# Optimization experiments

Hardware: AMD Instinct MI355X
Metric: run time of the kernel (lower is better)

The kernel has to match this reference:

```python
import jax, jax.numpy as jnp
import numpy as np
from jax import lax

ROUTING_ITERS = 3
EPS = 1e-8


def _conv(x, w, b, stride=1):
    # x: [B,C,H,W], w: [O,C,kh,kw]  (VALID padding, NCHW/OIHW)
    y = lax.conv_general_dilated(x, w, (stride, stride), 'VALID',
                                 dimension_numbers=('NCHW', 'OIHW', 'NCHW'))
    return y + b[None, :, None, None]


def _maxpool2(x):
    return lax.reduce_window(x, -jnp.inf, lax.max, (1, 1, 2, 2), (1, 1, 2, 2), 'VALID')


def _squash(s, axis=-1):
    n2 = jnp.sum(s * s, axis=axis, keepdims=True)
    return s * (n2 / (1.0 + n2)) / jnp.sqrt(n2 + EPS)


def setup_inputs() -> dict:
    key = jax.random.key(0)
    ks = jax.random.split(key, 9)
    p = lambda k, shp: (jax.random.normal(k, shp, dtype=jnp.float32) * 0.05)
    return {
        'x':  jax.random.normal(ks[0], (64, 1, 92, 92), dtype=jnp.float32),
        'w1': p(ks[1], (128, 1, 9, 9)),   'b1': jnp.zeros((128,), jnp.float32),
        'w2': p(ks[2], (64, 128, 5, 5)),  'b2': jnp.zeros((64,), jnp.float32),
        'wc': p(ks[3], (128, 64, 8, 8)),  'bc': jnp.zeros((128,), jnp.float32),
        # routing transform: [num_primary=1024, num_sar=10, out_dim=16, in_dim=32]
        'Wr': p(ks[4], (1024, 10, 16, 32)),
    }


def reference(x, w1, b1, w2, b2, wc, bc, Wr):
    B = x.shape[0]
    # feature extractor (dropout is identity at inference)
    h = jax.nn.relu(_conv(x, w1, b1))          # [B,128,84,84]
    h = _maxpool2(h)                            # [B,128,42,42]
    h = _conv(h, w2, b2)                        # [B,64,38,38]
    # primary capsule conv
    h = _conv(h, wc, bc, stride=2)              # [B,128,16,16]
    # 128 channels = 4 capsule types * 32-dim capsules, 16x16 spatial -> 1024 caps
    u = h.reshape(B, 4, 32, 16, 16).transpose(0, 1, 3, 4, 2).reshape(B, 1024, 32)
    u = _squash(u)                              # [B,1024,32]
    # u_hat: predictions of each primary cap for each SAR cap
    u_hat = jnp.einsum('bpi,ptoi->bpto', u, Wr)  # [B,1024,10,16]
    # dynamic routing
    b_log = jnp.zeros((B, 1024, 10), dtype=x.dtype)
    for _ in range(ROUTING_ITERS):
        c = jax.nn.softmax(b_log, axis=2)               # [B,1024,10]
        s = jnp.einsum('bpt,bpto->bto', c, u_hat)       # [B,10,16]
        v = _squash(s)                                   # [B,10,16]
        b_log = b_log + jnp.einsum('bpto,bto->bpt', u_hat, v)
    likelihood = jnp.sqrt(jnp.sum(v * v, axis=-1) + EPS)  # [B,10]
    return likelihood
```

## Files before the change

### kernel.cpp

```cpp
#include <hip/hip_runtime.h>
#include <hip/hip_bf16.h>
#include <math.h>


#define EPSF 1e-8f

typedef __bf16 bf16x8 __attribute__((ext_vector_type(8)));
typedef __bf16 bf16x4 __attribute__((ext_vector_type(4)));
typedef float floatx4 __attribute__((ext_vector_type(4)));
typedef float floatx16 __attribute__((ext_vector_type(16)));

__global__ __launch_bounds__(256) void k_t_all(const float* __restrict__ Wr,
                                               const float* __restrict__ wc,
                                               const float* __restrict__ w2,
                                               const float* __restrict__ w1,
                                               __bf16* __restrict__ wrb,
                                               __bf16* __restrict__ wca,
                                               __bf16* __restrict__ w2a,
                                               __bf16* __restrict__ w1b) {
    int i = blockIdx.x * 256 + threadIdx.x;
    if (i < 5242880) {
        int e = i & 7, l = (i >> 3) & 63;
        int pt_ = i >> 9;
        int o = l & 15, k = (l >> 4) * 8 + e;
        wrb[i] = (__bf16)Wr[((size_t)pt_ * 16 + o) * 32 + k];
        return;
    }
    int i2 = i - 5242880;
    if (i2 < 524288) {
        int j = i2 & 7, lane = (i2 >> 3) & 63, f = i2 >> 9;
        int ct = f & 3, ks = (f >> 2) & 1, khw = (f >> 3) & 63, icc = f >> 9;
        int c32 = lane & 31, h = lane >> 5;
        int oc = ct * 32 + c32;
        int ic = icc * 32 + ks * 16 + h * 8 + j;
        wca[i2] = (__bf16)wc[(oc * 64 + ic) * 64 + khw];
        return;
    }
    int i3 = i2 - 524288;
    if (i3 < 204800) {
        int j = i3 & 7, lane = (i3 >> 3) & 63, f = i3 >> 9;
        int mt = f & 1, ks = (f >> 1) & 3, rem = f >> 3;
        int khw = rem % 25, icc = rem / 25;
        int c32 = lane & 31, h = lane >> 5;
        int oc = mt * 32 + c32;
        int ic = icc * 64 + ks * 16 + h * 8 + j;
        w2a[i3] = (__bf16)w2[(oc * 128 + ic) * 25 + khw];
        return;
    }
    int i4 = i3 - 204800;
    if (i4 < 12288) {
        int kt = i4 >> 10, oc = (i4 >> 3) & 127, j = i4 & 7;
        int k = kt * 8 + j;
        w1b[i4] = (__bf16)(k < 81 ? w1[oc * 81 + k] : 0.f);
    }
}

__global__ __launch_bounds__(256, 3) void k_conv1_mfma(const float* __restrict__ x,
                                                       const __bf16* __restrict__ w1b,
                                                       const float* __restrict__ b1,
                                                       __bf16* __restrict__ h1n) {
    __shared__ float xs[960];
    __shared__ __bf16 Bl[18432];
    int py = blockIdx.x, b = blockIdx.y;
    int t = threadIdx.x;
    int lane = t & 63, w = t >> 6;
    int cc = lane & 15, q = lane >> 4;

    const float* xb = x + (size_t)b * 8464 + 2 * py * 92;
    for (int j = t; j < 920; j += 256) xs[j] = xb[j];

    bf16x8 af2[2][3];
#pragma unroll
    for (int g2 = 0; g2 < 2; ++g2)
#pragma unroll
        for (int ks = 0; ks < 3; ++ks)
            af2[g2][ks] = *(const bf16x8*)(w1b + ((ks * 4 + q) * 128 + g2 * 64 + w * 16 + cc) * 8);

    __syncthreads();

    if (t < 192) {
        int row = t / 96, pos = t - (t / 96) * 96;
        int sbase = row * 92 + pos;
        bool pvalid = pos < 84;
#pragma unroll
        for (int kt = 0; kt < 12; ++kt) {
            bf16x8 pk;
#pragma unroll
            for (int j = 0; j < 8; ++j) {
                int k = kt * 8 + j;
                int kh = k / 9, kw = k - kh * 9;
                float v = (pvalid && k < 81) ? xs[sbase + kh * 92 + kw] : 0.f;
                pk[j] = (__bf16)v;
            }
            *(bf16x8*)(Bl + ((kt * 2 + row) * 96 + pos) * 8) = pk;
        }
    }
    __syncthreads();

    floatx4 acc[2][2][6];
#pragma unroll
    for (int g2 = 0; g2 < 2; ++g2)
#pragma unroll
        for (int rr = 0; rr < 2; ++rr)
#pragma unroll
            for (int n6 = 0; n6 < 6; ++n6)
                acc[g2][rr][n6] = (floatx4){0.f, 0.f, 0.f, 0.f};

    const char* Bb = (const char*)Bl + cc * 16 + q * 3072;
#pragma unroll
    for (int rr = 0; rr < 2; ++rr)
#pragma unroll
        for (int n6 = 0; n6 < 6; ++n6) {
#pragma unroll
            for (int ks = 0; ks < 3; ++ks) {
                bf16x8 bf = *(const bf16x8*)(Bb + ks * 12288 + rr * 1536 + n6 * 256);
                acc[0][rr][n6] = __builtin_amdgcn_mfma_f32_16x16x32_bf16(af2[0][ks], bf, acc[0][rr][n6], 0, 0, 0);
                acc[1][rr][n6] = __builtin_amdgcn_mfma_f32_16x16x32_bf16(af2[1][ks], bf, acc[1][rr][n6], 0, 0, 0);
            }
        }

#pragma unroll
    for (int g2 = 0; g2 < 2; ++g2) {
        int oc0 = g2 * 64 + w * 16 + q * 4;
        float4 bv = *(const float4*)(b1 + oc0);
        size_t obase = (((size_t)b * 42 + py) * 42) * 128 + oc0;
#pragma unroll
        for (int n6 = 0; n6 < 6; ++n6) {
            bf16x4 pk;
#pragma unroll
            for (int r = 0; r < 4; ++r) {
                float vert = fmaxf(acc[g2][0][n6][r], acc[g2][1][n6][r]);
                float hz = fmaxf(vert, __shfl_xor(vert, 1, 64));
                float pooled = fmaxf(hz + ((const float*)&bv)[r], 0.f);
                pk[r] = (__bf16)pooled;
            }
            if ((cc & 1) == 0) {
                int px = n6 * 8 + (cc >> 1);
                if (px < 42)
                    *(bf16x4*)(h1n + obase + (size_t)px * 128) = pk;
            }
        }
    }
}

__global__ __launch_bounds__(256) void k_conv2(const __bf16* __restrict__ h1n,
                                               const __bf16* __restrict__ w2a,
                                               float* __restrict__ p01) {
    __shared__ __bf16 ins[25704];
    int g = blockIdx.x, b = blockIdx.y, icc = blockIdx.z;
    int row0 = g * 5;
    int t = threadIdx.x;
    int lane = t & 63, w = t >> 6;
    int c32 = lane & 31, h = lane >> 5;
    int validp = (g < 7) ? 190 : 114;
    int ic0 = icc * 64;

    int baseN[2], posi[2];
#pragma unroll
    for (int nt = 0; nt < 2; ++nt) {
        int pi = (w * 2 + nt) * 32 + c32;
        int pc = pi < validp ? pi : validp - 1;
        int r = pc / 38, c = pc - r * 38;
        posi[nt] = pi;
        baseN[nt] = (r * 42 + c) * 136 + h * 16;
    }

#pragma unroll
    for (int half = 0; half < 2; ++half) {
        uint4 rb[6];
        int lo[6];
#pragma unroll
        for (int k = 0; k < 6; ++k) {
            int j = (half * 6 + k) * 256 + t;
            if (j > 3023) j -= 256;
            int lr = j / 336, rem = j - lr * 336;
            int ix = rem >> 3, sb = rem & 7;
            int rg = row0 + lr; if (rg > 41) rg = 41;
            rb[k] = *(const uint4*)(h1n + ((((size_t)b * 42 + rg) * 42 + ix) * 128 + ic0 + sb * 8));
            lo[k] = (lr * 42 + ix) * 136 + sb * 16;
        }
#pragma unroll
        for (int k = 0; k < 6; ++k)
            *(uint4*)((char*)ins + lo[k]) = rb[k];
    }

    floatx16 acc[2][2];
#pragma unroll
    for (int mt = 0; mt < 2; ++mt)
#pragma unroll
        for (int nt = 0; nt < 2; ++nt)
#pragma unroll
            for (int i = 0; i < 16; ++i) acc[mt][nt][i] = 0.f;

    const __bf16* wic = w2a + (size_t)icc * 25 * 4096 + (lane << 3);

    bf16x8 abuf[3][8];
#pragma unroll
    for (int ks = 0; ks < 4; ++ks) {
        abuf[0][ks * 2]     = *(const bf16x8*)(wic + 0 * 4096 + ks * 1024);
        abuf[0][ks * 2 + 1] = *(const bf16x8*)(wic + 0 * 4096 + ks * 1024 + 512);
        abuf[1][ks * 2]     = *(const bf16x8*)(wic + 1 * 4096 + ks * 1024);
        abuf[1][ks * 2 + 1] = *(const bf16x8*)(wic + 1 * 4096 + ks * 1024 + 512);
    }

    __syncthreads();
#pragma unroll
    for (int khw = 0; khw < 25; ++khw) {
        if (khw + 2 < 25) {
            const __bf16* wk2 = wic + (khw + 2) * 4096;
#pragma unroll
            for (int ks = 0; ks < 4; ++ks) {
                abuf[(khw + 2) % 3][ks * 2]     = *(const bf16x8*)(wk2 + ks * 1024);
                abuf[(khw + 2) % 3][ks * 2 + 1] = *(const bf16x8*)(wk2 + ks * 1024 + 512);
            }
        }
        int kh = khw / 5, kw = khw - kh * 5;
        int doff = (kh * 42 + kw) * 136;
#pragma unroll
        for (int ks = 0; ks < 4; ++ks) {
            bf16x8 a0 = abuf[khw % 3][ks * 2];
            bf16x8 a1 = abuf[khw % 3][ks * 2 + 1];
#pragma unroll
            for (int nt = 0; nt < 2; ++nt) {
                bf16x8 bfr = *(const bf16x8*)((char*)ins + baseN[nt] + doff + ks * 32);
                acc[0][nt] = __builtin_amdgcn_mfma_f32_32x32x16_bf16(a0, bfr, acc[0][nt], 0, 0, 0);
                acc[1][nt] = __builtin_amdgcn_mfma_f32_32x32x16_bf16(a1, bfr, acc[1][nt], 0, 0, 0);
            }
        }
    }
    float* pdst = p01 + (size_t)icc * 5914624;
#pragma unroll
    for (int nt = 0; nt < 2; ++nt) {
        int pi = posi[nt];
        if (pi < validp) {
            int r = pi / 38, c = pi - r * 38;
            int oh = row0 + r;
            size_t obase = (((size_t)b * 38 + oh) * 38 + c) * 64;
#pragma unroll
            for (int mt = 0; mt < 2; ++mt) {
#pragma unroll
                for (int g2 = 0; g2 < 4; ++g2) {
                    int oc0 = mt * 32 + g2 * 8 + h * 4;
                    floatx4 pv;
                    pv[0] = acc[mt][nt][g2 * 4 + 0];
                    pv[1] = acc[mt][nt][g2 * 4 + 1];
                    pv[2] = acc[mt][nt][g2 * 4 + 2];
                    pv[3] = acc[mt][nt][g2 * 4 + 3];
                    *(floatx4*)(pdst + obase + oc0) = pv;
                }
            }
        }
    }
}

__global__ __launch_bounds__(256) void k_reduce_h2(const float* __restrict__ p01,
                                                   const float* __restrict__ b2,
                                                   __bf16* __restrict__ h2n) {
    int i = blockIdx.x * 256 + threadIdx.x;
    if (i >= 1478656) return;
    size_t e = (size_t)i * 4;
    floatx4 a = *(const floatx4*)(p01 + e);
    floatx4 b = *(const floatx4*)(p01 + 5914624 + e);
    floatx4 bv = *(const floatx4*)(b2 + ((i * 4) & 63));
    bf16x4 pk;
    pk.x = (__bf16)(a[0] + b[0] + bv[0]);
    pk.y = (__bf16)(a[1] + b[1] + bv[1]);
    pk.z = (__bf16)(a[2] + b[2] + bv[2]);
    pk.w = (__bf16)(a[3] + b[3] + bv[3]);
    *(bf16x4*)(h2n + e) = pk;
}

__global__ __launch_bounds__(256, 4) void k_convcaps(const __bf16* __restrict__ h2n,
                                                     const __bf16* __restrict__ wca,
                                                     float* __restrict__ pc) {
    __shared__ __bf16 ins[13680];
    int g = blockIdx.x, b = blockIdx.y, icc = blockIdx.z;
    int t = threadIdx.x;
    int lane = t & 63, ct = t >> 6;
    int c32 = lane & 31, h = lane >> 5;
    int rloc = c32 >> 4, cx = c32 & 15;
    int ic0 = icc * 32;

    floatx16 acc;
#pragma unroll
    for (int i = 0; i < 16; ++i) acc[i] = 0.f;

    int Bbase = (76 * rloc + cx) * 72 + h * 16;
    {
        uint4 rb[6];
        int lo[6];
#pragma unroll
        for (int k = 0; k < 6; ++k) {
            int j = k * 256 + t;
            if (j > 1519) j -= 256;
            int r = j / 152, rem = j - r * 152;
            int c = rem >> 2, s = rem & 3;
            rb[k] = *(const uint4*)(h2n + ((((size_t)b * 38 + 4 * g + r) * 38 + c) * 64 + ic0 + s * 8));
            int X = (r * 2 + (c & 1)) * 19 + (c >> 1);
            lo[k] = X * 72 + s * 16;
        }
#pragma unroll
        for (int k = 0; k < 6; ++k)
            *(uint4*)((char*)ins + lo[k]) = rb[k];
    }
    __syncthreads();
    const __bf16* wic = wca + ((size_t)icc * 64 * 8 + ct) * 512 + (lane << 3);
#pragma unroll
    for (int khw = 0; khw < 64; ++khw) {
        int kh = khw >> 3, kw = khw & 7;
        int par = kw & 1, k2 = kw >> 1;
        int doff = ((kh * 2 + par) * 19 + k2) * 72;
        const __bf16* wk = wic + khw * 4096;
#pragma unroll
        for (int ks = 0; ks < 2; ++ks) {
            bf16x8 af = *(const bf16x8*)(wk + ks * 2048);
            bf16x8 bfr = *(const bf16x8*)((char*)ins + Bbase + doff + ks * 32);
            acc = __builtin_amdgcn_mfma_f32_32x32x16_bf16(af, bfr, acc, 0, 0, 0);
        }
    }
    int pos = (2 * g + rloc) * 16 + cx;
    float* dst = pc + (size_t)icc * 2097152 + (((size_t)b * 1024 + ct * 256 + pos) * 32);
#pragma unroll
    for (int g2 = 0; g2 < 4; ++g2) {
        floatx4 pv;
        pv[0] = acc[g2 * 4 + 0];
        pv[1] = acc[g2 * 4 + 1];
        pv[2] = acc[g2 * 4 + 2];
        pv[3] = acc[g2 * 4 + 3];
        *(floatx4*)(dst + g2 * 8 + h * 4) = pv;
    }
}

__global__ __launch_bounds__(256) void k_squash(const float* __restrict__ pc,
                                                const float* __restrict__ bc,
                                                __bf16* __restrict__ ub) {
    int i = blockIdx.x * 256 + threadIdx.x;
    if (i >= 65536) return;
    int ct = (i >> 8) & 3;
    const float* p0 = pc + (size_t)i * 32;
    const float* p1 = pc + 2097152 + (size_t)i * 32;
    const float* bv = bc + ct * 32;
    float vals[32];
    float n2 = 0.f;
#pragma unroll
    for (int k = 0; k < 8; ++k) {
        floatx4 a = *(const floatx4*)(p0 + k * 4);
        floatx4 b = *(const floatx4*)(p1 + k * 4);
        floatx4 bb = *(const floatx4*)(bv + k * 4);
#pragma unroll
        for (int e = 0; e < 4; ++e) {
            float v = a[e] + b[e] + bb[e];
            vals[k * 4 + e] = v;
            n2 = fmaf(v, v, n2);
        }
    }
    float scale = (n2 / (1.f + n2)) / sqrtf(n2 + EPSF);
    __bf16* dst = ub + (size_t)i * 32;
#pragma unroll
    for (int k = 0; k < 8; ++k) {
        bf16x4 pk;
        pk.x = (__bf16)(vals[k * 4 + 0] * scale);
        pk.y = (__bf16)(vals[k * 4 + 1] * scale);
        pk.z = (__bf16)(vals[k * 4 + 2] * scale);
        pk.w = (__bf16)(vals[k * 4 + 3] * scale);
        *(bf16x4*)(dst + k * 4) = pk;
    }
}

__global__ __launch_bounds__(256) void k_uhat(const __bf16* __restrict__ ub,
                                              const __bf16* __restrict__ wrf,
                                              __bf16* __restrict__ uhT) {
    int pg = blockIdx.x, ts = blockIdx.y;
    int t = threadIdx.x;
    int lane = t & 63, bt = t >> 6;
    int bcol = bt * 16 + (lane & 15);
    int ko = lane >> 4;
    const __bf16* ubase = ub + (size_t)bcol * 32768 + ko * 8;
    __bf16* obase = uhT + ((size_t)bcol * 10 + ts) * 16384 + ko * 4;
#pragma unroll 4
    for (int i = 0; i < 16; ++i) {
        int p = pg * 16 + i;
        bf16x8 a = *(const bf16x8*)(wrf + (((size_t)p * 10 + ts) * 64 + lane) * 8);
        bf16x8 bb = *(const bf16x8*)(ubase + (size_t)p * 32);
        floatx4 c = (floatx4){0.f, 0.f, 0.f, 0.f};
        c = __builtin_amdgcn_mfma_f32_16x16x32_bf16(a, bb, c, 0, 0, 0);
        bf16x4 pk;
        pk.x = (__bf16)c[0];
        pk.y = (__bf16)c[1];
        pk.z = (__bf16)c[2];
        pk.w = (__bf16)c[3];
        *(bf16x4*)(obase + (size_t)p * 16) = pk;
    }
}

#define UHS_ADDR(P, HF) ((((P) << 5) + ((HF) << 4)) ^ ((((P) >> 2) & 7) << 4))
__global__ __launch_bounds__(256) void k_route(const __bf16* __restrict__ uhT,
                                               const float* __restrict__ blR,
                                               float* __restrict__ blW,
                                               float* __restrict__ out,
                                               int first, int dob, int last) {
    __shared__ __bf16 uh_s[16384];
    __shared__ float sred[4][16];
    __shared__ float vs[16];
    int b = blockIdx.x, tt = blockIdx.y;
    int t = threadIdx.x;
    const __bf16* uhb = uhT + ((size_t)b * 10 + tt) * 16384;
#pragma unroll
    for (int k = 0; k < 8; ++k) {
        int j = k * 256 + t;
        *(uint4*)((char*)uh_s + UHS_ADDR(j >> 1, j & 1)) =
            *(const uint4*)((const char*)uhb + j * 16);
    }
    __syncthreads();

    float acc[16];
#pragma unroll
    for (int o = 0; o < 16; ++o) acc[o] = 0.f;
    const float* blb = blR + b * 10240;
    for (int p = t; p < 1024; p += 256) {
        float c;
        if (first) {
            c = 0.1f;
        } else {
            float den = 0.f, et = 0.f;
#pragma unroll
            for (int tp = 0; tp < 10; ++tp) {
                float e = expf(blb[tp * 1024 + p]);
                den += e;
                if (tp == tt) et = e;
            }
            c = et / den;
        }
        bf16x8 u0 = *(const bf16x8*)((char*)uh_s + UHS_ADDR(p, 0));
        bf16x8 u1 = *(const bf16x8*)((char*)uh_s + UHS_ADDR(p, 1));
#pragma unroll
        for (int o = 0; o < 8; ++o) {
            acc[o]     = fmaf(c, (float)u0[o], acc[o]);
            acc[8 + o] = fmaf(c, (float)u1[o], acc[8 + o]);
        }
    }
    int lane = t & 63, wid = t >> 6;
#pragma unroll
    for (int o = 0; o < 16; ++o) {
        float v = acc[o];
#pragma unroll
        for (int off = 32; off >= 1; off >>= 1) v += __shfl_xor(v, off, 64);
        if (lane == 0) sred[wid][o] = v;
    }
    __syncthreads();
    if (t < 16) {
        float s = (sred[0][t] + sred[1][t]) + (sred[2][t] + sred[3][t]);
        float n2 = s * s;
#pragma unroll
        for (int off = 1; off < 16; off <<= 1) n2 += __shfl_xor(n2, off, 16);
        float scale = (n2 / (1.f + n2)) / sqrtf(n2 + EPSF);
        vs[t] = s * scale;
        if (last && t == 0) {
            float sv2 = n2 * scale * scale;
            out[b * 10 + tt] = sqrtf(sv2 + EPSF);
        }
    }
    __syncthreads();

    if (dob) {
        const float* blr = blR + (b * 10 + tt) * 1024;
        float* blw = blW + (b * 10 + tt) * 1024;
        for (int p = t; p < 1024; p += 256) {
            bf16x8 u0 = *(const bf16x8*)((char*)uh_s + UHS_ADDR(p, 0));
            bf16x8 u1 = *(const bf16x8*)((char*)uh_s + UHS_ADDR(p, 1));
            float d = 0.f;
#pragma unroll
            for (int o = 0; o < 8; ++o) {
                d = fmaf((float)u0[o], vs[o], d);
                d = fmaf((float)u1[o], vs[8 + o], d);
            }
            blw[p] = first ? d : (blr[p] + d);
        }
    }
}

extern "C" void kernel_launch(void* const* d_in, const int* in_sizes, int n_in,
                              void* d_out, int out_size, void* d_ws, size_t ws_size,
                              hipStream_t stream) {
    const float* x  = (const float*)d_in[0];
    const float* w1 = (const float*)d_in[1];
    const float* b1 = (const float*)d_in[2];
    const float* w2 = (const float*)d_in[3];
    const float* b2 = (const float*)d_in[4];
    const float* wc = (const float*)d_in[5];
    const float* bc = (const float*)d_in[6];
    const float* Wr = (const float*)d_in[7];
    float* out = (float*)d_out;
    float* ws  = (float*)d_ws;

    __bf16* w2a = (__bf16*)(ws);
    __bf16* wca = (__bf16*)(ws + 102400);
    __bf16* w1b = (__bf16*)(ws + 364544);
    __bf16* h1n = (__bf16*)(ws + 375040);
    __bf16* h2n = (__bf16*)(ws + 7600384);
    __bf16* ub  = (__bf16*)(ws + 12654848);
    float*  blA = ws + 14752000;
    __bf16* wrb = (__bf16*)(ws + 15417600);
    float*  p01 = ws + 18039040;
    float*  pc  = ws + 18039040;
    float*  blB = ws + 29868288;
    __bf16* uhT = (__bf16*)(ws + 375040);

    k_t_all<<<23376, 256, 0, stream>>>(Wr, wc, w2, w1, wrb, wca, w2a, w1b);
    k_conv1_mfma<<<dim3(42, 64), 256, 0, stream>>>(x, w1b, b1, h1n);
    k_conv2<<<dim3(8, 64, 2), 256, 0, stream>>>(h1n, w2a, p01);
    k_reduce_h2<<<5776, 256, 0, stream>>>(p01, b2, h2n);
    k_convcaps<<<dim3(8, 64, 2), 256, 0, stream>>>(h2n, wca, pc);
    k_squash<<<256, 256, 0, stream>>>(pc, bc, ub);
    k_uhat<<<dim3(64, 10), 256, 0, stream>>>(ub, wrb, uhT);
    k_route<<<dim3(64, 10), 256, 0, stream>>>(uhT, blA, blA, out, 1, 1, 0);
    k_route<<<dim3(64, 10), 256, 0, stream>>>(uhT, blA, blB, out, 0, 1, 0);
    k_route<<<dim3(64, 10), 256, 0, stream>>>(uhT, blB, blB, out, 0, 0, 1);
}
```

Baseline: 273.4 us.

## Fuse three routing iterations into one cooperative kernel with grid sync

Merges the three k_route launches into a single cooperative kernel that loads each block's u_hat slice into shared memory once and runs all three routing iterations, using a grid-wide sync between iterations to exchange the routing logits. This removes two kernel launches and two reloads of the 32KB u_hat tile per block. In exchange it requires all 640 blocks to be co-resident and adds grid barrier overhead. Correctness depends on the cooperative launch succeeding.

```diff
diff --git a/kernel.cpp b/kernel.cpp
--- a/kernel.cpp
+++ b/kernel.cpp
@@ -1,5 +1,6 @@
 #include <hip/hip_runtime.h>
 #include <hip/hip_bf16.h>
+#include <hip/hip_cooperative_groups.h>
 #include <math.h>
 
 
@@ -394,16 +395,17 @@
 }
 
 #define UHS_ADDR(P, HF) ((((P) << 5) + ((HF) << 4)) ^ ((((P) >> 2) & 7) << 4))
-__global__ __launch_bounds__(256) void k_route(const __bf16* __restrict__ uhT,
-                                               const float* __restrict__ blR,
-                                               float* __restrict__ blW,
-                                               float* __restrict__ out,
-                                               int first, int dob, int last) {
+__global__ __launch_bounds__(256) void k_route_all(const __bf16* __restrict__ uhT,
+                                                   float* __restrict__ blA,
+                                                   float* __restrict__ blB,
+                                                   float* __restrict__ out) {
+    cooperative_groups::grid_group gg = cooperative_groups::this_grid();
     __shared__ __bf16 uh_s[16384];
     __shared__ float sred[4][16];
     __shared__ float vs[16];
     int b = blockIdx.x, tt = blockIdx.y;
     int t = threadIdx.x;
+    int lane = t & 63, wid = t >> 6;
     const __bf16* uhb = uhT + ((size_t)b * 10 + tt) * 16384;
 #pragma unroll
     for (int k = 0; k < 8; ++k) {
@@ -413,68 +415,74 @@
     }
     __syncthreads();
 
-    float acc[16];
-#pragma unroll
-    for (int o = 0; o < 16; ++o) acc[o] = 0.f;
-    const float* blb = blR + b * 10240;
-    for (int p = t; p < 1024; p += 256) {
-        float c;
-        if (first) {
-            c = 0.1f;
-        } else {
-            float den = 0.f, et = 0.f;
-#pragma unroll
-            for (int tp = 0; tp < 10; ++tp) {
-                float e = expf(blb[tp * 1024 + p]);
-                den += e;
-                if (tp == tt) et = e;
-            }
-            c = et / den;
-        }
-        bf16x8 u0 = *(const bf16x8*)((char*)uh_s + UHS_ADDR(p, 0));
-        bf16x8 u1 = *(const bf16x8*)((char*)uh_s + UHS_ADDR(p, 1));
-#pragma unroll
-        for (int o = 0; o < 8; ++o) {
-            acc[o]     = fmaf(c, (float)u0[o], acc[o]);
-            acc[8 + o] = fmaf(c, (float)u1[o], acc[8 + o]);
-        }
-    }
-    int lane = t & 63, wid = t >> 6;
-#pragma unroll
-    for (int o = 0; o < 16; ++o) {
-        float v = acc[o];
-#pragma unroll
-        for (int off = 32; off >= 1; off >>= 1) v += __shfl_xor(v, off, 64);
-        if (lane == 0) sred[wid][o] = v;
-    }
-    __syncthreads();
-    if (t < 16) {
-        float s = (sred[0][t] + sred[1][t]) + (sred[2][t] + sred[3][t]);
-        float n2 = s * s;
-#pragma unroll
-        for (int off = 1; off < 16; off <<= 1) n2 += __shfl_xor(n2, off, 16);
-        float scale = (n2 / (1.f + n2)) / sqrtf(n2 + EPSF);
-        vs[t] = s * scale;
-        if (last && t == 0) {
-            float sv2 = n2 * scale * scale;
-            out[b * 10 + tt] = sqrtf(sv2 + EPSF);
-        }
-    }
-    __syncthreads();
-
-    if (dob) {
-        const float* blr = blR + (b * 10 + tt) * 1024;
-        float* blw = blW + (b * 10 + tt) * 1024;
+#pragma unroll 1
+    for (int it = 0; it < 3; ++it) {
+        const float* blR = (it == 1) ? blA : blB;
+        float acc[16];
+#pragma unroll
+        for (int o = 0; o < 16; ++o) acc[o] = 0.f;
+        const float* blb = blR + b * 10240;
         for (int p = t; p < 1024; p += 256) {
+            float c;
+            if (it == 0) {
+                c = 0.1f;
+            } else {
+                float den = 0.f, et = 0.f;
+#pragma unroll
+                for (int tp = 0; tp < 10; ++tp) {
+                    float e = expf(blb[tp * 1024 + p]);
+                    den += e;
+                    if (tp == tt) et = e;
+                }
+                c = et / den;
+            }
             bf16x8 u0 = *(const bf16x8*)((char*)uh_s + UHS_ADDR(p, 0));
             bf16x8 u1 = *(const bf16x8*)((char*)uh_s + UHS_ADDR(p, 1));
-            float d = 0.f;
 #pragma unroll
             for (int o = 0; o < 8; ++o) {
-                d = fmaf((float)u0[o], vs[o], d);
-                d = fmaf((float)u1[o], vs[8 + o], d);
-            }
-            blw[p] = first ? d : (blr[p] + d);
+                acc[o]     = fmaf(c, (float)u0[o], acc[o]);
+                acc[8 + o] = fmaf(c, (float)u1[o], acc[8 + o]);
+            }
+        }
+#pragma unroll
+        for (int o = 0; o < 16; ++o) {
+            float v = acc[o];
+#pragma unroll
+            for (int off = 32; off >= 1; off >>= 1) v += __shfl_xor(v, off, 64);
+            if (lane == 0) sred[wid][o] = v;
+        }
+        __syncthreads();
+        if (t < 16) {
+            float s = (sred[0][t] + sred[1][t]) + (sred[2][t] + sred[3][t]);
+            float n2 = s * s;
+#pragma unroll
+            for (int off = 1; off < 16; off <<= 1) n2 += __shfl_xor(n2, off, 16);
+            float scale = (n2 / (1.f + n2)) / sqrtf(n2 + EPSF);
+            vs[t] = s * scale;
+            if (it == 2 && t == 0) {
+                float sv2 = n2 * scale * scale;
+                out[b * 10 + tt] = sqrtf(sv2 + EPSF);
+            }
+        }
+        __syncthreads();
+
+        if (it < 2) {
+            float* blw = (it == 0) ? blA : blB;
+            const float* blr = blA + (b * 10 + tt) * 1024;
+            float* blwp = blw + (b * 10 + tt) * 1024;
+            for (int p = t; p < 1024; p += 256) {
+                bf16x8 u0 = *(const bf16x8*)((char*)uh_s + UHS_ADDR(p, 0));
+                bf16x8 u1 = *(const bf16x8*)((char*)uh_s + UHS_ADDR(p, 1));
+                float d = 0.f;
+#pragma unroll
+                for (int o = 0; o < 8; ++o) {
+                    d = fmaf((float)u0[o], vs[o], d);
+                    d = fmaf((float)u1[o], vs[8 + o], d);
+                }
+                blwp[p] = (it == 0) ? d : (blr[p] + d);
+            }
+            __threadfence();
+            gg.sync();
         }
     }
 }
@@ -513,7 +521,10 @@
     k_convcaps<<<dim3(8, 64, 2), 256, 0, stream>>>(h2n, wca, pc);
     k_squash<<<256, 256, 0, stream>>>(pc, bc, ub);
     k_uhat<<<dim3(64, 10), 256, 0, stream>>>(ub, wrb, uhT);
-    k_route<<<dim3(64, 10), 256, 0, stream>>>(uhT, blA, blA, out, 1, 1, 0);
-    k_route<<<dim3(64, 10), 256, 0, stream>>>(uhT, blA, blB, out, 0, 1, 0);
-    k_route<<<dim3(64, 10), 256, 0, stream>>>(uhT, blB, blB, out, 0, 0, 1);
-}
+    {
+        const __bf16* uhTc = uhT;
+        void* args[] = {(void*)&uhTc, (void*)&blA, (void*)&blB, (void*)&out};
+        hipLaunchCooperativeKernel((void*)k_route_all, dim3(64, 10), dim3(256),
+                                   args, 0, stream);
+    }
+}
```

Result: slower. 542.9 us (+98.6%).
